# Optimization experiments

Hardware: AMD Instinct MI355X
Metric: run time of the kernel (lower is better)

The kernel has to match this reference:

```python
import jax, jax.numpy as jnp
import numpy as np

B, D, H, C = 131072, 256, 256, 8
TAU = 0.15


def setup_inputs() -> dict:
    key = jax.random.key(0)
    ks = jax.random.split(key, 10)
    s_in = 1.0 / np.sqrt(D)
    s_h = 1.0 / np.sqrt(H)
    return {
        "x": jax.random.normal(ks[0], (B, D), jnp.float32),
        # root node params
        "W1": jax.random.normal(ks[1], (D, H), jnp.float32) * s_in,
        "b1": jnp.zeros((H,), jnp.float32),
        "W2": jax.random.normal(ks[2], (H, C), jnp.float32) * s_h,
        "b2": jnp.zeros((C,), jnp.float32),
        # one leaf child per class: stacked params [C, ...]
        "Wc1": jax.random.normal(ks[3], (C, H, H), jnp.float32) * s_h,
        "bc1": jnp.zeros((C, H), jnp.float32),
        "Wc2": jax.random.normal(ks[4], (C, H, C), jnp.float32) * s_h,
        "bc2": jnp.zeros((C, C), jnp.float32),
        "tau": jnp.full((C,), TAU, jnp.float32),
    }


def reference(x, W1, b1, W2, b2, Wc1, bc1, Wc2, bc2, tau):
    # root dense + head
    h = jax.nn.relu(x @ W1 + b1)            # [B, H]
    logits = h @ W2 + b2                    # [B, C]
    probs = jax.nn.softmax(logits, axis=1)  # [B, C]

    # route(): walk classes in descending prob order, take the first class
    # that has a child (all C do here) and whose prob >= tau[class].
    # Equivalent vectorized form: argmax of probs restricted to passing classes.
    mask = probs >= tau                     # [B, C]
    routed = jnp.any(mask, axis=1)          # [B]
    masked = jnp.where(mask, probs, -1.0)
    best = jnp.argmax(masked, axis=1)       # [B] chosen child per sample

    out_logits, out_h = logits, h
    for c in range(C):                      # small fixed expert loop
        sel = (routed & (best == c))[:, None]
        h_c = jax.nn.relu(h @ Wc1[c] + bc1[c])  # [B, H]
        l_c = h_c @ Wc2[c] + bc2[c]             # [B, C]
        out_logits = jnp.where(sel, l_c, out_logits)
        out_h = jnp.where(sel, h_c, out_h)

    depths = routed.astype(jnp.int32)       # leaf children => depth 1, else 0
    return out_logits, out_h, depths
```

## Files before the change

kernel.cpp:

```cpp
#include <hip/hip_runtime.h>

#define Bn 131072
#define Dn 256
#define Hn 256
#define Cn 8

typedef __attribute__((ext_vector_type(4))) float f32x4;
typedef __attribute__((ext_vector_type(8))) __bf16 bf16x8;

#define LDA 40

__device__ inline unsigned short rtn_bf16(float v) {
    unsigned int u = __float_as_uint(v);
    unsigned int r = u + 0x7fffu + ((u >> 16) & 1u);
    return (unsigned short)(r >> 16);
}
__device__ inline float bf16_to_f(unsigned short h) {
    return __uint_as_float((unsigned int)h << 16);
}
__device__ inline void split3(float v, unsigned short& a0, unsigned short& a1,
                              unsigned short& a2) {
    a0 = rtn_bf16(v); float r = v - bf16_to_f(a0);
    a1 = rtn_bf16(r); r -= bf16_to_f(a1);
    a2 = rtn_bf16(r);
}
__device__ inline ushort4 cvt4(float4 v) {
    return make_ushort4(rtn_bf16(v.x), rtn_bf16(v.y), rtn_bf16(v.z), rtn_bf16(v.w));
}

__global__ __launch_bounds__(256)
void prep_kernel(const float* __restrict__ W1, const float* __restrict__ Wc1,
                 unsigned short* __restrict__ W1t0, unsigned short* __restrict__ W1t1,
                 unsigned short* __restrict__ W1t2, unsigned short* __restrict__ Wc1t)
{
    const int idx = blockIdx.x * 256 + threadIdx.x;
    if (idx < 65536) {
        const int n = idx >> 8, k = idx & 255;
        unsigned short a0, a1, a2;
        split3(W1[k * 256 + n], a0, a1, a2);
        W1t0[idx] = a0; W1t1[idx] = a1; W1t2[idx] = a2;
    } else {
        const int j = idx - 65536;
        const int e = j >> 16, rem = j & 65535;
        const int n = rem >> 8, k = rem & 255;
        Wc1t[(e << 16) + n * 256 + k] = rtn_bf16(Wc1[(e << 16) + k * 256 + n]);
    }
}

__global__ __launch_bounds__(512, 4)
void root_kernel(const float* __restrict__ x,
                 const unsigned short* __restrict__ Wt0,
                 const unsigned short* __restrict__ Wt1,
                 const unsigned short* __restrict__ Wt2,
                 const float* __restrict__ b1, const float* __restrict__ W2,
                 const float* __restrict__ b2, const float* __restrict__ tau,
                 float* __restrict__ out_logits, float* __restrict__ out_h,
                 float* __restrict__ out_depth, int* __restrict__ cnt,
                 int* __restrict__ lists)
{
    __shared__ unsigned short sA0[128 * LDA], sA1[128 * LDA], sA2[128 * LDA];
    __shared__ float sP[128][8];
    __shared__ int   sCnt[8], sBase[8], sBest[128], sSlot[128];

    const int t    = threadIdx.x;
    const int lane = t & 63;
    const int w    = t >> 6;
    const int tx   = lane & 15;
    const int q    = lane >> 4;
    const long r0  = (long)blockIdx.x * 128;

    if (t < 8) sCnt[t] = 0;
    ((float*)sP)[t] = 0.0f;
    ((float*)sP)[t + 512] = 0.0f;

    const int colA = w * 32 + tx;
    const int colB = colA + 16;
    const unsigned short* bp0 = Wt0 + colA * 256 + q * 8;
    const unsigned short* bp1 = Wt1 + colA * 256 + q * 8;
    const unsigned short* bp2 = Wt2 + colA * 256 + q * 8;
    const unsigned short* bp3 = Wt0 + colB * 256 + q * 8;
    const unsigned short* bp4 = Wt1 + colB * 256 + q * 8;
    const unsigned short* bp5 = Wt2 + colB * 256 + q * 8;

    f32x4 acc[8][2];
#pragma unroll
    for (int mt = 0; mt < 8; mt++)
#pragma unroll
        for (int nt = 0; nt < 2; nt++) acc[mt][nt] = (f32x4)0.0f;

    const int ar = t >> 3, ak = t & 7;
    const float4* xr0 = (const float4*)x + (r0 + ar) * 64 + ak;
    const float4* xr1 = (const float4*)x + (r0 + 64 + ar) * 64 + ak;
    float4 xv0 = xr0[0];
    float4 xv1 = xr1[0];

    for (int i = 0; i < 8; i++) {
        if (i) __syncthreads();
        {
            unsigned short h0[4], h1[4], h2[4];
            split3(xv0.x, h0[0], h1[0], h2[0]);
            split3(xv0.y, h0[1], h1[1], h2[1]);
            split3(xv0.z, h0[2], h1[2], h2[2]);
            split3(xv0.w, h0[3], h1[3], h2[3]);
            *(ushort4*)&sA0[ar * LDA + ak * 4] = make_ushort4(h0[0], h0[1], h0[2], h0[3]);
            *(ushort4*)&sA1[ar * LDA + ak * 4] = make_ushort4(h1[0], h1[1], h1[2], h1[3]);
            *(ushort4*)&sA2[ar * LDA + ak * 4] = make_ushort4(h2[0], h2[1], h2[2], h2[3]);
            split3(xv1.x, h0[0], h1[0], h2[0]);
            split3(xv1.y, h0[1], h1[1], h2[1]);
            split3(xv1.z, h0[2], h1[2], h2[2]);
            split3(xv1.w, h0[3], h1[3], h2[3]);
            *(ushort4*)&sA0[(64 + ar) * LDA + ak * 4] = make_ushort4(h0[0], h0[1], h0[2], h0[3]);
            *(ushort4*)&sA1[(64 + ar) * LDA + ak * 4] = make_ushort4(h1[0], h1[1], h1[2], h1[3]);
            *(ushort4*)&sA2[(64 + ar) * LDA + ak * 4] = make_ushort4(h2[0], h2[1], h2[2], h2[3]);
        }
        if (i < 7) { xv0 = xr0[(i + 1) * 8]; xv1 = xr1[(i + 1) * 8]; }
        __syncthreads();

        const int ko = i * 32;
        const bf16x8 B0 = *(const bf16x8*)(bp0 + ko);
        const bf16x8 B1 = *(const bf16x8*)(bp1 + ko);
        const bf16x8 B2 = *(const bf16x8*)(bp2 + ko);
        const bf16x8 B3 = *(const bf16x8*)(bp3 + ko);
        const bf16x8 B4 = *(const bf16x8*)(bp4 + ko);
        const bf16x8 B5 = *(const bf16x8*)(bp5 + ko);

#pragma unroll
        for (int mt = 0; mt < 8; mt++) {
            const bf16x8 A0 = *(const bf16x8*)&sA0[(mt * 16 + tx) * LDA + q * 8];
            const bf16x8 A1 = *(const bf16x8*)&sA1[(mt * 16 + tx) * LDA + q * 8];
            const bf16x8 A2 = *(const bf16x8*)&sA2[(mt * 16 + tx) * LDA + q * 8];
            acc[mt][0] = __builtin_amdgcn_mfma_f32_16x16x32_bf16(A0, B0, acc[mt][0], 0, 0, 0);
            acc[mt][0] = __builtin_amdgcn_mfma_f32_16x16x32_bf16(A0, B1, acc[mt][0], 0, 0, 0);
            acc[mt][0] = __builtin_amdgcn_mfma_f32_16x16x32_bf16(A1, B0, acc[mt][0], 0, 0, 0);
            acc[mt][0] = __builtin_amdgcn_mfma_f32_16x16x32_bf16(A1, B1, acc[mt][0], 0, 0, 0);
            acc[mt][0] = __builtin_amdgcn_mfma_f32_16x16x32_bf16(A0, B2, acc[mt][0], 0, 0, 0);
            acc[mt][0] = __builtin_amdgcn_mfma_f32_16x16x32_bf16(A2, B0, acc[mt][0], 0, 0, 0);
            acc[mt][1] = __builtin_amdgcn_mfma_f32_16x16x32_bf16(A0, B3, acc[mt][1], 0, 0, 0);
            acc[mt][1] = __builtin_amdgcn_mfma_f32_16x16x32_bf16(A0, B4, acc[mt][1], 0, 0, 0);
            acc[mt][1] = __builtin_amdgcn_mfma_f32_16x16x32_bf16(A1, B3, acc[mt][1], 0, 0, 0);
            acc[mt][1] = __builtin_amdgcn_mfma_f32_16x16x32_bf16(A1, B4, acc[mt][1], 0, 0, 0);
            acc[mt][1] = __builtin_amdgcn_mfma_f32_16x16x32_bf16(A0, B5, acc[mt][1], 0, 0, 0);
            acc[mt][1] = __builtin_amdgcn_mfma_f32_16x16x32_bf16(A2, B3, acc[mt][1], 0, 0, 0);
        }
    }

    const float b1c0 = b1[colA], b1c1 = b1[colB];
    float w20[8], w21[8];
    {
        const float4 a0 = ((const float4*)W2)[colA * 2];
        const float4 a1 = ((const float4*)W2)[colA * 2 + 1];
        const float4 c0 = ((const float4*)W2)[colB * 2];
        const float4 c1 = ((const float4*)W2)[colB * 2 + 1];
        w20[0]=a0.x; w20[1]=a0.y; w20[2]=a0.z; w20[3]=a0.w;
        w20[4]=a1.x; w20[5]=a1.y; w20[6]=a1.z; w20[7]=a1.w;
        w21[0]=c0.x; w21[1]=c0.y; w21[2]=c0.z; w21[3]=c0.w;
        w21[4]=c1.x; w21[5]=c1.y; w21[6]=c1.z; w21[7]=c1.w;
    }

#pragma unroll
    for (int mt = 0; mt < 8; mt++) {
        float pm[4][8];
#pragma unroll
        for (int reg = 0; reg < 4; reg++) {
            const float h0 = fmaxf(acc[mt][0][reg] + b1c0, 0.0f);
            const float h1 = fmaxf(acc[mt][1][reg] + b1c1, 0.0f);
            const int row = mt * 16 + q * 4 + reg;
            out_h[(r0 + row) * 256 + colA] = h0;
            out_h[(r0 + row) * 256 + colB] = h1;
#pragma unroll
            for (int c = 0; c < 8; c++)
                pm[reg][c] = h0 * w20[c] + h1 * w21[c];
        }
#pragma unroll
        for (int reg = 0; reg < 4; reg++)
#pragma unroll
            for (int c = 0; c < 8; c++) {
                float v = pm[reg][c];
                v += __shfl_xor(v, 1, 16);
                v += __shfl_xor(v, 2, 16);
                v += __shfl_xor(v, 4, 16);
                v += __shfl_xor(v, 8, 16);
                if (tx == 0) atomicAdd(&sP[mt * 16 + q * 4 + reg][c], v);
            }
    }
    __syncthreads();

    if (t < 128) {
        const long row = r0 + t;
        float l[8];
        float mx = -1e30f;
#pragma unroll
        for (int c = 0; c < 8; c++) {
            l[c] = sP[t][c] + b2[c];
            mx = fmaxf(mx, l[c]);
        }
        float e[8], s = 0.0f;
#pragma unroll
        for (int c = 0; c < 8; c++) { e[c] = expf(l[c] - mx); s += e[c]; }
        const float inv = 1.0f / s;
        int best = 0; float bp = -1.0f;
#pragma unroll
        for (int c = 0; c < 8; c++) {
            const float pr = e[c] * inv;
            const float m  = (pr >= tau[c]) ? pr : -1.0f;
            if (m > bp) { bp = m; best = c; }
        }
        const bool routed = (bp >= 0.0f);
        float4* lo4 = (float4*)&out_logits[row * 8];
        lo4[0] = make_float4(l[0], l[1], l[2], l[3]);
        lo4[1] = make_float4(l[4], l[5], l[6], l[7]);
        out_depth[row] = routed ? 1.0f : 0.0f;
        if (routed) {
            sSlot[t] = atomicAdd(&sCnt[best], 1);
            sBest[t] = best;
        } else {
            sBest[t] = -1;
        }
    }
    __syncthreads();
    if (t < 8) sBase[t] = sCnt[t] ? atomicAdd(&cnt[t], sCnt[t]) : 0;
    __syncthreads();
    if (t < 128 && sBest[t] >= 0) {
        const int e = sBest[t];
        lists[(long)e * Bn + sBase[e] + sSlot[t]] = (int)(r0 + t);
    }
}

__global__ __launch_bounds__(512, 4)
void expert_kernel(const unsigned short* __restrict__ Wc1t,
                   const float* __restrict__ bc1,
                   const float* __restrict__ Wc2, const float* __restrict__ bc2,
                   float* __restrict__ out_logits, float* __restrict__ out_h,
                   const int* __restrict__ cnt, const int* __restrict__ lists)
{
    const int e = blockIdx.y;
    const int n = cnt[e];
    const int tile0 = blockIdx.x * 128;
    if (tile0 >= n) return;
    const int nrows = min(128, n - tile0);

    __shared__ unsigned short sA[2][128 * LDA];
    __shared__ float sP[128][8];
    __shared__ int   sRidx[128];

    const int t    = threadIdx.x;
    const int lane = t & 63;
    const int w    = t >> 6;
    const int tx   = lane & 15;
    const int q    = lane >> 4;

    if (t < 128) sRidx[t] = lists[(long)e * Bn + tile0 + min(t, nrows - 1)];
    ((float*)sP)[t] = 0.0f;
    ((float*)sP)[t + 512] = 0.0f;

    const unsigned short* W = Wc1t + (long)e * 65536;
    const int colA = w * 32 + tx;
    const int colB = colA + 16;
    const unsigned short* bpA = W + colA * 256 + q * 8;
    const unsigned short* bpB = W + colB * 256 + q * 8;

    f32x4 acc[8][2];
#pragma unroll
    for (int mt = 0; mt < 8; mt++)
#pragma unroll
        for (int nt = 0; nt < 2; nt++) acc[mt][nt] = (f32x4)0.0f;

    const int ar = t >> 3, ak = t & 7;
    __syncthreads();
    const float4* hr0 = (const float4*)out_h + (long)sRidx[ar] * 64 + ak;
    const float4* hr1 = (const float4*)out_h + (long)sRidx[64 + ar] * 64 + ak;

    float4 xv0 = hr0[0], xv1 = hr1[0];
    *(ushort4*)&sA[0][ar * LDA + ak * 4]        = cvt4(xv0);
    *(ushort4*)&sA[0][(64 + ar) * LDA + ak * 4] = cvt4(xv1);
    xv0 = hr0[8]; xv1 = hr1[8];
    bf16x8 BcA = *(const bf16x8*)(bpA);
    bf16x8 BcB = *(const bf16x8*)(bpB);
    __syncthreads();

#pragma unroll 2
    for (int i = 0; i < 8; i++) {
        const int cur = i & 1;
        if (i < 7) {
            *(ushort4*)&sA[cur ^ 1][ar * LDA + ak * 4]        = cvt4(xv0);
            *(ushort4*)&sA[cur ^ 1][(64 + ar) * LDA + ak * 4] = cvt4(xv1);
            if (i < 6) { xv0 = hr0[(i + 2) * 8]; xv1 = hr1[(i + 2) * 8]; }
        }
        bf16x8 BnA, BnB;
        if (i < 7) {
            BnA = *(const bf16x8*)(bpA + (i + 1) * 32);
            BnB = *(const bf16x8*)(bpB + (i + 1) * 32);
        }
#pragma unroll
        for (int mt = 0; mt < 8; mt++) {
            const bf16x8 A = *(const bf16x8*)&sA[cur][(mt * 16 + tx) * LDA + q * 8];
            acc[mt][0] = __builtin_amdgcn_mfma_f32_16x16x32_bf16(A, BcA, acc[mt][0], 0, 0, 0);
            acc[mt][1] = __builtin_amdgcn_mfma_f32_16x16x32_bf16(A, BcB, acc[mt][1], 0, 0, 0);
        }
        if (i < 7) { BcA = BnA; BcB = BnB; }
        __syncthreads();
    }

    const float* bc1e = bc1 + (long)e * Hn;
    const float b1c0 = bc1e[colA], b1c1 = bc1e[colB];
    const float* W2c = Wc2 + (long)e * Hn * Cn;
    float w20[8], w21[8];
    {
        const float4 a0 = ((const float4*)W2c)[colA * 2];
        const float4 a1 = ((const float4*)W2c)[colA * 2 + 1];
        const float4 c0 = ((const float4*)W2c)[colB * 2];
        const float4 c1 = ((const float4*)W2c)[colB * 2 + 1];
        w20[0]=a0.x; w20[1]=a0.y; w20[2]=a0.z; w20[3]=a0.w;
        w20[4]=a1.x; w20[5]=a1.y; w20[6]=a1.z; w20[7]=a1.w;
        w21[0]=c0.x; w21[1]=c0.y; w21[2]=c0.z; w21[3]=c0.w;
        w21[4]=c1.x; w21[5]=c1.y; w21[6]=c1.z; w21[7]=c1.w;
    }

#pragma unroll
    for (int mt = 0; mt < 8; mt++) {
        float pm[4][8];
#pragma unroll
        for (int reg = 0; reg < 4; reg++) {
            const float h0 = fmaxf(acc[mt][0][reg] + b1c0, 0.0f);
            const float h1 = fmaxf(acc[mt][1][reg] + b1c1, 0.0f);
            const int row = mt * 16 + q * 4 + reg;
            if (row < nrows) {
                out_h[(long)sRidx[row] * 256 + colA] = h0;
                out_h[(long)sRidx[row] * 256 + colB] = h1;
            }
#pragma unroll
            for (int c = 0; c < 8; c++)
                pm[reg][c] = h0 * w20[c] + h1 * w21[c];
        }
#pragma unroll
        for (int reg = 0; reg < 4; reg++)
#pragma unroll
            for (int c = 0; c < 8; c++) {
                float v = pm[reg][c];
                v += __shfl_xor(v, 1, 16);
                v += __shfl_xor(v, 2, 16);
                v += __shfl_xor(v, 4, 16);
                v += __shfl_xor(v, 8, 16);
                if (tx == 0) atomicAdd(&sP[mt * 16 + q * 4 + reg][c], v);
            }
    }
    __syncthreads();

    if (t < nrows) {
        const long row = sRidx[t];
        const float* bc2e = bc2 + (long)e * Cn;
        float4* lo4 = (float4*)&out_logits[row * 8];
        lo4[0] = make_float4(sP[t][0] + bc2e[0], sP[t][1] + bc2e[1],
                             sP[t][2] + bc2e[2], sP[t][3] + bc2e[3]);
        lo4[1] = make_float4(sP[t][4] + bc2e[4], sP[t][5] + bc2e[5],
                             sP[t][6] + bc2e[6], sP[t][7] + bc2e[7]);
    }
}

extern "C" void kernel_launch(void* const* d_in, const int* in_sizes, int n_in,
                              void* d_out, int out_size, void* d_ws, size_t ws_size,
                              hipStream_t stream)
{
    const float* x   = (const float*)d_in[0];
    const float* W1  = (const float*)d_in[1];
    const float* b1  = (const float*)d_in[2];
    const float* W2  = (const float*)d_in[3];
    const float* b2  = (const float*)d_in[4];
    const float* Wc1 = (const float*)d_in[5];
    const float* bc1 = (const float*)d_in[6];
    const float* Wc2 = (const float*)d_in[7];
    const float* bc2 = (const float*)d_in[8];
    const float* tau = (const float*)d_in[9];

    float* out_logits = (float*)d_out;
    float* out_h      = out_logits + (long)Bn * Cn;
    float* out_depth  = out_h + (long)Bn * Hn;

    char* wsb = (char*)d_ws;
    int* cnt   = (int*)wsb;
    int* lists = (int*)(wsb + 128);
    unsigned short* W1t0 = (unsigned short*)(wsb + 128 + (size_t)8 * Bn * 4);
    unsigned short* W1t1 = W1t0 + 65536;
    unsigned short* W1t2 = W1t1 + 65536;
    unsigned short* Wc1t = W1t2 + 65536;

    hipMemsetAsync(d_ws, 0, 128, stream);

    prep_kernel<<<dim3((65536 + 8 * 65536) / 256), 256, 0, stream>>>(
        W1, Wc1, W1t0, W1t1, W1t2, Wc1t);

    root_kernel<<<dim3(Bn / 128), 512, 0, stream>>>(
        x, W1t0, W1t1, W1t2, b1, W2, b2, tau, out_logits, out_h, out_depth,
        cnt, lists);

    expert_kernel<<<dim3(Bn / 128, 8), 512, 0, stream>>>(
        Wc1t, bc1, Wc2, bc2, out_logits, out_h, cnt, lists);
}
```

Before: 624.8 us.

## Double-buffer root GEMM A tiles and prefetch x two stages ahead

The root kernel's shared-memory A tiles (three bf16 split components) become double-buffered. The next K-slice is split and staged into the alternate buffer while MFMAs consume the current one, and global x loads are prefetched two iterations ahead. This cuts each iteration from two barriers to one and hides load latency behind compute. In exchange it doubles A-tile LDS use, which may limit the 4-blocks-per-CU occupancy target, and adds register pressure from the extra prefetched float4s.

```diff
diff --git a/kernel.cpp b/kernel.cpp
--- a/kernel.cpp
+++ b/kernel.cpp
@@ -58,7 +58,8 @@
                  float* __restrict__ out_depth, int* __restrict__ cnt,
                  int* __restrict__ lists)
 {
-    __shared__ unsigned short sA0[128 * LDA], sA1[128 * LDA], sA2[128 * LDA];
+    __shared__ unsigned short sA0[2][128 * LDA], sA1[2][128 * LDA],
+                              sA2[2][128 * LDA];
     __shared__ float sP[128][8];
     __shared__ int   sCnt[8], sBase[8], sBest[128], sSlot[128];
 
@@ -91,32 +92,36 @@
     const int ar = t >> 3, ak = t & 7;
     const float4* xr0 = (const float4*)x + (r0 + ar) * 64 + ak;
     const float4* xr1 = (const float4*)x + (r0 + 64 + ar) * 64 + ak;
-    float4 xv0 = xr0[0];
-    float4 xv1 = xr1[0];
+
+    auto stage = [&](int b, float4 v0, float4 v1) {
+        unsigned short h0[4], h1[4], h2[4];
+        split3(v0.x, h0[0], h1[0], h2[0]);
+        split3(v0.y, h0[1], h1[1], h2[1]);
+        split3(v0.z, h0[2], h1[2], h2[2]);
+        split3(v0.w, h0[3], h1[3], h2[3]);
+        *(ushort4*)&sA0[b][ar * LDA + ak * 4] = make_ushort4(h0[0], h0[1], h0[2], h0[3]);
+        *(ushort4*)&sA1[b][ar * LDA + ak * 4] = make_ushort4(h1[0], h1[1], h1[2], h1[3]);
+        *(ushort4*)&sA2[b][ar * LDA + ak * 4] = make_ushort4(h2[0], h2[1], h2[2], h2[3]);
+        split3(v1.x, h0[0], h1[0], h2[0]);
+        split3(v1.y, h0[1], h1[1], h2[1]);
+        split3(v1.z, h0[2], h1[2], h2[2]);
+        split3(v1.w, h0[3], h1[3], h2[3]);
+        *(ushort4*)&sA0[b][(64 + ar) * LDA + ak * 4] = make_ushort4(h0[0], h0[1], h0[2], h0[3]);
+        *(ushort4*)&sA1[b][(64 + ar) * LDA + ak * 4] = make_ushort4(h1[0], h1[1], h1[2], h1[3]);
+        *(ushort4*)&sA2[b][(64 + ar) * LDA + ak * 4] = make_ushort4(h2[0], h2[1], h2[2], h2[3]);
+    };
+
+    {
+        float4 v0 = xr0[0], v1 = xr1[0];
+        stage(0, v0, v1);
+    }
+    float4 pa0 = xr0[8],  pa1 = xr1[8];
+    float4 pb0 = xr0[16], pb1 = xr1[16];
+    __syncthreads();
 
     for (int i = 0; i < 8; i++) {
-        if (i) __syncthreads();
-        {
-            unsigned short h0[4], h1[4], h2[4];
-            split3(xv0.x, h0[0], h1[0], h2[0]);
-            split3(xv0.y, h0[1], h1[1], h2[1]);
-            split3(xv0.z, h0[2], h1[2], h2[2]);
-            split3(xv0.w, h0[3], h1[3], h2[3]);
-            *(ushort4*)&sA0[ar * LDA + ak * 4] = make_ushort4(h0[0], h0[1], h0[2], h0[3]);
-            *(ushort4*)&sA1[ar * LDA + ak * 4] = make_ushort4(h1[0], h1[1], h1[2], h1[3]);
-            *(ushort4*)&sA2[ar * LDA + ak * 4] = make_ushort4(h2[0], h2[1], h2[2], h2[3]);
-            split3(xv1.x, h0[0], h1[0], h2[0]);
-            split3(xv1.y, h0[1], h1[1], h2[1]);
-            split3(xv1.z, h0[2], h1[2], h2[2]);
-            split3(xv1.w, h0[3], h1[3], h2[3]);
-            *(ushort4*)&sA0[(64 + ar) * LDA + ak * 4] = make_ushort4(h0[0], h0[1], h0[2], h0[3]);
-            *(ushort4*)&sA1[(64 + ar) * LDA + ak * 4] = make_ushort4(h1[0], h1[1], h1[2], h1[3]);
-            *(ushort4*)&sA2[(64 + ar) * LDA + ak * 4] = make_ushort4(h2[0], h2[1], h2[2], h2[3]);
-        }
-        if (i < 7) { xv0 = xr0[(i + 1) * 8]; xv1 = xr1[(i + 1) * 8]; }
-        __syncthreads();
-
-        const int ko = i * 32;
+        const int cur = i & 1;
+        const int ko  = i * 32;
         const bf16x8 B0 = *(const bf16x8*)(bp0 + ko);
         const bf16x8 B1 = *(const bf16x8*)(bp1 + ko);
         const bf16x8 B2 = *(const bf16x8*)(bp2 + ko);
@@ -124,11 +129,17 @@
         const bf16x8 B4 = *(const bf16x8*)(bp4 + ko);
         const bf16x8 B5 = *(const bf16x8*)(bp5 + ko);
 
+        if (i < 7) {
+            stage(cur ^ 1, pa0, pa1);
+            pa0 = pb0; pa1 = pb1;
+            if (i < 5) { pb0 = xr0[(i + 3) * 8]; pb1 = xr1[(i + 3) * 8]; }
+        }
+
 #pragma unroll
         for (int mt = 0; mt < 8; mt++) {
-            const bf16x8 A0 = *(const bf16x8*)&sA0[(mt * 16 + tx) * LDA + q * 8];
-            const bf16x8 A1 = *(const bf16x8*)&sA1[(mt * 16 + tx) * LDA + q * 8];
-            const bf16x8 A2 = *(const bf16x8*)&sA2[(mt * 16 + tx) * LDA + q * 8];
+            const bf16x8 A0 = *(const bf16x8*)&sA0[cur][(mt * 16 + tx) * LDA + q * 8];
+            const bf16x8 A1 = *(const bf16x8*)&sA1[cur][(mt * 16 + tx) * LDA + q * 8];
+            const bf16x8 A2 = *(const bf16x8*)&sA2[cur][(mt * 16 + tx) * LDA + q * 8];
             acc[mt][0] = __builtin_amdgcn_mfma_f32_16x16x32_bf16(A0, B0, acc[mt][0], 0, 0, 0);
             acc[mt][0] = __builtin_amdgcn_mfma_f32_16x16x32_bf16(A0, B1, acc[mt][0], 0, 0, 0);
             acc[mt][0] = __builtin_amdgcn_mfma_f32_16x16x32_bf16(A1, B0, acc[mt][0], 0, 0, 0);
@@ -142,6 +153,7 @@
             acc[mt][1] = __builtin_amdgcn_mfma_f32_16x16x32_bf16(A0, B5, acc[mt][1], 0, 0, 0);
             acc[mt][1] = __builtin_amdgcn_mfma_f32_16x16x32_bf16(A2, B3, acc[mt][1], 0, 0, 0);
         }
+        __syncthreads();
     }
 
     const float b1c0 = b1[colA], b1c1 = b1[colB];
```

Result: slower. 675.6 us (+8.1%).

## Fuse expert routing and expert MLP into root kernel per 128-row tile

Applied to the files above, without the earlier changes.

Merges the root and expert kernels so each block routes its own 128 rows locally, builds per-expert 16-row tasks in shared memory, and runs the expert MLP per wave directly. This removes the global atomic lists, the memset, a kernel launch, and the expert kernel's strided gather of rows from global memory. In exchange each 16-row task reloads the full 256x256 expert weight slice from global/L2 with no LDS staging, reads h back from out_h just written, and partially filled tasks waste MFMA work.

```diff
diff --git a/kernel.cpp b/kernel.cpp
--- a/kernel.cpp
+++ b/kernel.cpp
@@ -48,19 +48,22 @@
 }
 
 __global__ __launch_bounds__(512, 4)
-void root_kernel(const float* __restrict__ x,
-                 const unsigned short* __restrict__ Wt0,
-                 const unsigned short* __restrict__ Wt1,
-                 const unsigned short* __restrict__ Wt2,
-                 const float* __restrict__ b1, const float* __restrict__ W2,
-                 const float* __restrict__ b2, const float* __restrict__ tau,
-                 float* __restrict__ out_logits, float* __restrict__ out_h,
-                 float* __restrict__ out_depth, int* __restrict__ cnt,
-                 int* __restrict__ lists)
+void fused_kernel(const float* __restrict__ x,
+                  const unsigned short* __restrict__ Wt0,
+                  const unsigned short* __restrict__ Wt1,
+                  const unsigned short* __restrict__ Wt2,
+                  const float* __restrict__ b1, const float* __restrict__ W2,
+                  const float* __restrict__ b2, const float* __restrict__ tau,
+                  const unsigned short* __restrict__ Wc1t,
+                  const float* __restrict__ bc1,
+                  const float* __restrict__ Wc2, const float* __restrict__ bc2,
+                  float* __restrict__ out_logits, float* __restrict__ out_h,
+                  float* __restrict__ out_depth)
 {
     __shared__ unsigned short sA0[128 * LDA], sA1[128 * LDA], sA2[128 * LDA];
     __shared__ float sP[128][8];
-    __shared__ int   sCnt[8], sBase[8], sBest[128], sSlot[128];
+    __shared__ int   sCnt[8], sOff[8], sBest[128], sSlot[128], sOrd[128];
+    __shared__ int   sTaskE[16], sTaskM[16], sNT;
 
     const int t    = threadIdx.x;
     const int lane = t & 63;
@@ -206,154 +209,132 @@
             if (m > bp) { bp = m; best = c; }
         }
         const bool routed = (bp >= 0.0f);
-        float4* lo4 = (float4*)&out_logits[row * 8];
-        lo4[0] = make_float4(l[0], l[1], l[2], l[3]);
-        lo4[1] = make_float4(l[4], l[5], l[6], l[7]);
         out_depth[row] = routed ? 1.0f : 0.0f;
         if (routed) {
             sSlot[t] = atomicAdd(&sCnt[best], 1);
             sBest[t] = best;
         } else {
             sBest[t] = -1;
-        }
-    }
-    __syncthreads();
-    if (t < 8) sBase[t] = sCnt[t] ? atomicAdd(&cnt[t], sCnt[t]) : 0;
-    __syncthreads();
-    if (t < 128 && sBest[t] >= 0) {
-        const int e = sBest[t];
-        lists[(long)e * Bn + sBase[e] + sSlot[t]] = (int)(r0 + t);
-    }
-}
-
-__global__ __launch_bounds__(512, 4)
-void expert_kernel(const unsigned short* __restrict__ Wc1t,
-                   const float* __restrict__ bc1,
-                   const float* __restrict__ Wc2, const float* __restrict__ bc2,
-                   float* __restrict__ out_logits, float* __restrict__ out_h,
-                   const int* __restrict__ cnt, const int* __restrict__ lists)
-{
-    const int e = blockIdx.y;
-    const int n = cnt[e];
-    const int tile0 = blockIdx.x * 128;
-    if (tile0 >= n) return;
-    const int nrows = min(128, n - tile0);
-
-    __shared__ unsigned short sA[2][128 * LDA];
-    __shared__ float sP[128][8];
-    __shared__ int   sRidx[128];
-
-    const int t    = threadIdx.x;
-    const int lane = t & 63;
-    const int w    = t >> 6;
-    const int tx   = lane & 15;
-    const int q    = lane >> 4;
-
-    if (t < 128) sRidx[t] = lists[(long)e * Bn + tile0 + min(t, nrows - 1)];
+            float4* lo4 = (float4*)&out_logits[row * 8];
+            lo4[0] = make_float4(l[0], l[1], l[2], l[3]);
+            lo4[1] = make_float4(l[4], l[5], l[6], l[7]);
+        }
+    }
+    __syncthreads();
+
     ((float*)sP)[t] = 0.0f;
     ((float*)sP)[t + 512] = 0.0f;
-
-    const unsigned short* W = Wc1t + (long)e * 65536;
-    const int colA = w * 32 + tx;
-    const int colB = colA + 16;
-    const unsigned short* bpA = W + colA * 256 + q * 8;
-    const unsigned short* bpB = W + colB * 256 + q * 8;
-
-    f32x4 acc[8][2];
-#pragma unroll
-    for (int mt = 0; mt < 8; mt++)
-#pragma unroll
-        for (int nt = 0; nt < 2; nt++) acc[mt][nt] = (f32x4)0.0f;
-
-    const int ar = t >> 3, ak = t & 7;
-    __syncthreads();
-    const float4* hr0 = (const float4*)out_h + (long)sRidx[ar] * 64 + ak;
-    const float4* hr1 = (const float4*)out_h + (long)sRidx[64 + ar] * 64 + ak;
-
-    float4 xv0 = hr0[0], xv1 = hr1[0];
-    *(ushort4*)&sA[0][ar * LDA + ak * 4]        = cvt4(xv0);
-    *(ushort4*)&sA[0][(64 + ar) * LDA + ak * 4] = cvt4(xv1);
-    xv0 = hr0[8]; xv1 = hr1[8];
-    bf16x8 BcA = *(const bf16x8*)(bpA);
-    bf16x8 BcB = *(const bf16x8*)(bpB);
-    __syncthreads();
-
-#pragma unroll 2
-    for (int i = 0; i < 8; i++) {
-        const int cur = i & 1;
-        if (i < 7) {
-            *(ushort4*)&sA[cur ^ 1][ar * LDA + ak * 4]        = cvt4(xv0);
-            *(ushort4*)&sA[cur ^ 1][(64 + ar) * LDA + ak * 4] = cvt4(xv1);
-            if (i < 6) { xv0 = hr0[(i + 2) * 8]; xv1 = hr1[(i + 2) * 8]; }
-        }
-        bf16x8 BnA, BnB;
-        if (i < 7) {
-            BnA = *(const bf16x8*)(bpA + (i + 1) * 32);
-            BnB = *(const bf16x8*)(bpB + (i + 1) * 32);
-        }
-#pragma unroll
-        for (int mt = 0; mt < 8; mt++) {
-            const bf16x8 A = *(const bf16x8*)&sA[cur][(mt * 16 + tx) * LDA + q * 8];
-            acc[mt][0] = __builtin_amdgcn_mfma_f32_16x16x32_bf16(A, BcA, acc[mt][0], 0, 0, 0);
-            acc[mt][1] = __builtin_amdgcn_mfma_f32_16x16x32_bf16(A, BcB, acc[mt][1], 0, 0, 0);
-        }
-        if (i < 7) { BcA = BnA; BcB = BnB; }
-        __syncthreads();
-    }
-
-    const float* bc1e = bc1 + (long)e * Hn;
-    const float b1c0 = bc1e[colA], b1c1 = bc1e[colB];
-    const float* W2c = Wc2 + (long)e * Hn * Cn;
-    float w20[8], w21[8];
-    {
-        const float4 a0 = ((const float4*)W2c)[colA * 2];
-        const float4 a1 = ((const float4*)W2c)[colA * 2 + 1];
-        const float4 c0 = ((const float4*)W2c)[colB * 2];
-        const float4 c1 = ((const float4*)W2c)[colB * 2 + 1];
-        w20[0]=a0.x; w20[1]=a0.y; w20[2]=a0.z; w20[3]=a0.w;
-        w20[4]=a1.x; w20[5]=a1.y; w20[6]=a1.z; w20[7]=a1.w;
-        w21[0]=c0.x; w21[1]=c0.y; w21[2]=c0.z; w21[3]=c0.w;
-        w21[4]=c1.x; w21[5]=c1.y; w21[6]=c1.z; w21[7]=c1.w;
-    }
-
-#pragma unroll
-    for (int mt = 0; mt < 8; mt++) {
-        float pm[4][8];
+    if (t == 0) {
+        int off = 0, T = 0;
+        for (int e = 0; e < 8; e++) {
+            sOff[e] = off;
+            const int n = sCnt[e];
+            for (int m = 0; m * 16 < n; m++) { sTaskE[T] = e; sTaskM[T] = m; T++; }
+            off += n;
+        }
+        sNT = T;
+    }
+    __syncthreads();
+    if (t < 128 && sBest[t] >= 0)
+        sOrd[sOff[sBest[t]] + sSlot[t]] = t;
+    __syncthreads();
+
+    for (int task = w; task < sNT; task += 8) {
+        const int e   = sTaskE[task];
+        const int m0  = sTaskM[task] << 4;
+        const int ce  = sCnt[e];
+        const int be  = sOff[e];
+        const int my  = m0 + tx;
+        const int lr  = sOrd[be + (my < ce ? my : 0)];
+        const float4* hrow = (const float4*)out_h + (r0 + lr) * 64 + q * 2;
+
+        int  orow[4]; bool oval[4];
 #pragma unroll
         for (int reg = 0; reg < 4; reg++) {
-            const float h0 = fmaxf(acc[mt][0][reg] + b1c0, 0.0f);
-            const float h1 = fmaxf(acc[mt][1][reg] + b1c1, 0.0f);
-            const int row = mt * 16 + q * 4 + reg;
-            if (row < nrows) {
-                out_h[(long)sRidx[row] * 256 + colA] = h0;
-                out_h[(long)sRidx[row] * 256 + colB] = h1;
+            const int rr = m0 + q * 4 + reg;
+            oval[reg] = rr < ce;
+            orow[reg] = oval[reg] ? sOrd[be + rr] : 0;
+        }
+
+        bf16x8 Af[8];
+#pragma unroll
+        for (int j = 0; j < 8; j++) {
+            const float4 u0 = hrow[j * 8];
+            const float4 u1 = hrow[j * 8 + 1];
+            union { bf16x8 v; ushort4 u[2]; } pk;
+            pk.u[0] = cvt4(u0); pk.u[1] = cvt4(u1);
+            Af[j] = pk.v;
+        }
+
+        const unsigned short* We = Wc1t + (e << 16);
+        const float* bc1e = bc1 + (e << 8);
+        const float* w2e  = Wc2 + e * (Hn * Cn);
+
+#pragma unroll
+        for (int half = 0; half < 2; half++) {
+            const int cb = half << 7;
+            f32x4 ac[8];
+#pragma unroll
+            for (int nt = 0; nt < 8; nt++) ac[nt] = (f32x4)0.0f;
+
+#pragma unroll
+            for (int kh = 0; kh < 2; kh++) {
+#pragma unroll
+                for (int nt = 0; nt < 8; nt++) {
+                    const unsigned short* bp = We + (cb + nt * 16 + tx) * 256 + kh * 128 + q * 8;
+#pragma unroll
+                    for (int j = 0; j < 4; j++) {
+                        const bf16x8 Bf = *(const bf16x8*)(bp + j * 32);
+                        ac[nt] = __builtin_amdgcn_mfma_f32_16x16x32_bf16(Af[kh * 4 + j], Bf, ac[nt], 0, 0, 0);
+                    }
+                }
             }
-#pragma unroll
-            for (int c = 0; c < 8; c++)
-                pm[reg][c] = h0 * w20[c] + h1 * w21[c];
-        }
-#pragma unroll
-        for (int reg = 0; reg < 4; reg++)
-#pragma unroll
-            for (int c = 0; c < 8; c++) {
-                float v = pm[reg][c];
-                v += __shfl_xor(v, 1, 16);
-                v += __shfl_xor(v, 2, 16);
-                v += __shfl_xor(v, 4, 16);
-                v += __shfl_xor(v, 8, 16);
-                if (tx == 0) atomicAdd(&sP[mt * 16 + q * 4 + reg][c], v);
+
+            float pm[4][8];
+#pragma unroll
+            for (int reg = 0; reg < 4; reg++)
+#pragma unroll
+                for (int c = 0; c < 8; c++) pm[reg][c] = 0.0f;
+
+#pragma unroll
+            for (int nt = 0; nt < 8; nt++) {
+                const int col = cb + nt * 16 + tx;
+                const float bb = bc1e[col];
+                const float4 wa = ((const float4*)w2e)[col * 2];
+                const float4 wb = ((const float4*)w2e)[col * 2 + 1];
+#pragma unroll
+                for (int reg = 0; reg < 4; reg++) {
+                    const float hc = fmaxf(ac[nt][reg] + bb, 0.0f);
+                    if (oval[reg])
+                        out_h[(r0 + orow[reg]) * 256 + col] = hc;
+                    pm[reg][0] += hc * wa.x; pm[reg][1] += hc * wa.y;
+                    pm[reg][2] += hc * wa.z; pm[reg][3] += hc * wa.w;
+                    pm[reg][4] += hc * wb.x; pm[reg][5] += hc * wb.y;
+                    pm[reg][6] += hc * wb.z; pm[reg][7] += hc * wb.w;
+                }
             }
-    }
-    __syncthreads();
-
-    if (t < nrows) {
-        const long row = sRidx[t];
-        const float* bc2e = bc2 + (long)e * Cn;
-        float4* lo4 = (float4*)&out_logits[row * 8];
-        lo4[0] = make_float4(sP[t][0] + bc2e[0], sP[t][1] + bc2e[1],
-                             sP[t][2] + bc2e[2], sP[t][3] + bc2e[3]);
-        lo4[1] = make_float4(sP[t][4] + bc2e[4], sP[t][5] + bc2e[5],
-                             sP[t][6] + bc2e[6], sP[t][7] + bc2e[7]);
+#pragma unroll
+            for (int reg = 0; reg < 4; reg++)
+#pragma unroll
+                for (int c = 0; c < 8; c++) {
+                    float v = pm[reg][c];
+                    v += __shfl_xor(v, 1, 16);
+                    v += __shfl_xor(v, 2, 16);
+                    v += __shfl_xor(v, 4, 16);
+                    v += __shfl_xor(v, 8, 16);
+                    if (tx == 0 && oval[reg]) atomicAdd(&sP[orow[reg]][c], v);
+                }
+        }
+    }
+    __syncthreads();
+
+    if (t < 128 && sBest[t] >= 0) {
+        const float* b2e = bc2 + sBest[t] * Cn;
+        float4* lo4 = (float4*)&out_logits[(r0 + t) * 8];
+        lo4[0] = make_float4(sP[t][0] + b2e[0], sP[t][1] + b2e[1],
+                             sP[t][2] + b2e[2], sP[t][3] + b2e[3]);
+        lo4[1] = make_float4(sP[t][4] + b2e[4], sP[t][5] + b2e[5],
+                             sP[t][6] + b2e[6], sP[t][7] + b2e[7]);
     }
 }
 
@@ -377,22 +358,15 @@
     float* out_depth  = out_h + (long)Bn * Hn;
 
     char* wsb = (char*)d_ws;
-    int* cnt   = (int*)wsb;
-    int* lists = (int*)(wsb + 128);
-    unsigned short* W1t0 = (unsigned short*)(wsb + 128 + (size_t)8 * Bn * 4);
+    unsigned short* W1t0 = (unsigned short*)wsb;
     unsigned short* W1t1 = W1t0 + 65536;
     unsigned short* W1t2 = W1t1 + 65536;
     unsigned short* Wc1t = W1t2 + 65536;
 
-    hipMemsetAsync(d_ws, 0, 128, stream);
-
     prep_kernel<<<dim3((65536 + 8 * 65536) / 256), 256, 0, stream>>>(
         W1, Wc1, W1t0, W1t1, W1t2, Wc1t);
 
-    root_kernel<<<dim3(Bn / 128), 512, 0, stream>>>(
-        x, W1t0, W1t1, W1t2, b1, W2, b2, tau, out_logits, out_h, out_depth,
-        cnt, lists);
-
-    expert_kernel<<<dim3(Bn / 128, 8), 512, 0, stream>>>(
-        Wc1t, bc1, Wc2, bc2, out_logits, out_h, cnt, lists);
-}
+    fused_kernel<<<dim3(Bn / 128), 512, 0, stream>>>(
+        x, W1t0, W1t1, W1t2, b1, W2, b2, tau, Wc1t, bc1, Wc2, bc2,
+        out_logits, out_h, out_depth);
+}
```

Result: slower. 802.1 us (+28.4%).
